# Optimization experiments

Measured on AMD Instinct MI355X. Metric: run time of the kernel, lower is better.

The kernel has to match this reference:

```python
import jax, jax.numpy as jnp
import numpy as np

N = 4096          # number of bodies
DIM = 2           # 2D physics (Parallax robot soccer)
K_BROAD = 4 * N   # broad phase keeps first 4N AABB overlaps (per source)
K_EXACT = N       # exact phase keeps first N true penetrations (per source)


def setup_inputs() -> dict:
    key = jax.random.key(0)
    k1, k2 = jax.random.split(key)
    # disk bodies scattered in a ~160x160 arena -> dense enough for many hits
    pos = jax.random.normal(k1, (N, DIM), dtype=jnp.float32) * 40.0
    radius = jax.random.uniform(k2, (N,), dtype=jnp.float32, minval=0.5, maxval=1.5)
    return {"pos": pos, "radius": radius}


def _forward(pos, radius):
    n = pos.shape[0]
    # ---- broad phase: sphere AABB = pos +- radius; two boxes overlap iff
    # |p_i - p_j| <= r_i + r_j on every axis. Full O(N^2) scan (as in source),
    # compact the first K_BROAD hits in row-major (i*n + j) order.
    d = jnp.abs(pos[:, None, :] - pos[None, :, :])            # [N,N,DIM]
    rsum = radius[:, None] + radius[None, :]                  # [N,N]
    overlap = jnp.all(d <= rsum[..., None], axis=-1)          # [N,N] bool
    overlap = overlap & ~jnp.eye(n, dtype=bool)               # skip self-pairs
    flat = overlap.reshape(-1)                                # [N*N]
    rank = jnp.cumsum(flat.astype(jnp.int32)) - 1             # slot of each hit
    valid = flat & (rank < K_BROAD)
    slot = jnp.where(valid, rank, K_BROAD)                    # K_BROAD -> dropped
    ii = jnp.repeat(jnp.arange(n, dtype=jnp.int32), n)
    jj = jnp.tile(jnp.arange(n, dtype=jnp.int32), n)
    bi = jnp.full((K_BROAD,), -1, jnp.int32).at[slot].set(ii, mode='drop')
    bj = jnp.full((K_BROAD,), -1, jnp.int32).at[slot].set(jj, mode='drop')
    # ---- exact phase: sphere-sphere penetration test on broad pairs,
    # keep first K_EXACT real penetrations (gather-compute-compact).
    gi = jnp.clip(bi, 0, n - 1)
    gj = jnp.clip(bj, 0, n - 1)
    dv = pos[gi] - pos[gj]                                    # [K_BROAD,DIM]
    dist = jnp.sqrt(jnp.sum(dv * dv, axis=-1) + 1e-12)
    pen_depth = radius[gi] + radius[gj] - dist                # >0 means overlap
    hit = (bi >= 0) & (pen_depth > 0)
    erank = jnp.cumsum(hit.astype(jnp.int32)) - 1
    evalid = hit & (erank < K_EXACT)
    eslot = jnp.where(evalid, erank, K_EXACT)                 # K_EXACT -> dropped
    pen_vec = dv * (pen_depth / dist)[:, None]                # penetration vector
    ei = jnp.full((K_EXACT,), -1, jnp.int32).at[eslot].set(bi, mode='drop')
    ej = jnp.full((K_EXACT,), -1, jnp.int32).at[eslot].set(bj, mode='drop')
    ev = jnp.zeros((K_EXACT, pos.shape[-1]), pos.dtype).at[eslot].set(pen_vec, mode='drop')
    # ---- resolve: each body of the pair is pushed half the penetration apart,
    si = jnp.where(ei >= 0, ei, n)                            # n -> dropped
    sj = jnp.where(ej >= 0, ej, n)
    new_i = pos[jnp.clip(ei, 0, n - 1)] + 0.5 * ev
    new_j = pos[jnp.clip(ej, 0, n - 1)] - 0.5 * ev
    out = pos.at[si].set(new_i, mode='drop')
    out = out.at[sj].set(new_j, mode='drop')
    return out


def reference(pos, radius):
    return _forward(pos, radius)
```

## Files before the change

kernel.cpp:

```cpp
#include <hip/hip_runtime.h>

#define NB 4096
#define KBROAD (4 * NB)
#define KEXACT NB
typedef unsigned long long u64;

__global__ __launch_bounds__(256) void count_kernel(
    const float2* __restrict__ pos, const float* __restrict__ rad,
    int* __restrict__ row_counts, u64* __restrict__ masks,
    int* __restrict__ last_key) {
  int gid = blockIdx.x * blockDim.x + threadIdx.x;
  if (gid < NB) last_key[gid] = -1;
  int wave = gid >> 6;
  int lane = gid & 63;
  int r0 = wave * 2;
  float2 p0 = pos[r0], p1 = pos[r0 + 1];
  float ra0 = rad[r0], ra1 = rad[r0 + 1];
  int cc = r0 >> 6;
  u64 mw0 = 0, mw1 = 0;
  int c0 = 0, c1 = 0;
  for (int c = 0; c < 64; ++c) {
    int j = c * 64 + lane;
    float2 pj = pos[j];
    float rj = rad[j];
    bool h0 = fmaxf(fabsf(p0.x - pj.x), fabsf(p0.y - pj.y)) <= (ra0 + rj);
    bool h1 = fmaxf(fabsf(p1.x - pj.x), fabsf(p1.y - pj.y)) <= (ra1 + rj);
    u64 m0 = __ballot(h0);
    u64 m1 = __ballot(h1);
    if (c == cc) {
      m0 &= ~(1ull << (r0 & 63));
      m1 &= ~(1ull << ((r0 + 1) & 63));
    }
    if (lane == c) { mw0 = m0; mw1 = m1; }
    c0 += __popcll(m0);
    c1 += __popcll(m1);
  }
  masks[(size_t)r0 * 64 + lane] = mw0;
  masks[(size_t)(r0 + 1) * 64 + lane] = mw1;
  if (lane == 0) { row_counts[r0] = c0; row_counts[r0 + 1] = c1; }
}

__global__ __launch_bounds__(256) void fill_kernel(
    const float2* __restrict__ pos, const float* __restrict__ rad,
    const int* __restrict__ row_counts, const u64* __restrict__ masks,
    float2* __restrict__ penvec, unsigned* __restrict__ pij,
    int* __restrict__ totalp) {
  __shared__ int rb[NB];
  __shared__ int wsum[4];
  int t = threadIdx.x;
  int wv = t >> 6, lane = t & 63;
  int c[16], s = 0;
  const int4* rc4 = (const int4*)row_counts;
  #pragma unroll
  for (int k4 = 0; k4 < 4; ++k4) {
    int4 d = rc4[t * 4 + k4];
    c[4 * k4 + 0] = d.x; c[4 * k4 + 1] = d.y;
    c[4 * k4 + 2] = d.z; c[4 * k4 + 3] = d.w;
    s += d.x + d.y + d.z + d.w;
  }
  int v = s;
  #pragma unroll
  for (int off = 1; off < 64; off <<= 1) {
    int u = __shfl_up(v, off);
    if (lane >= off) v += u;
  }
  if (lane == 63) wsum[wv] = v;
  __syncthreads();
  int wbase = 0;
  #pragma unroll
  for (int w = 0; w < 4; ++w) if (w < wv) wbase += wsum[w];
  int run = wbase + v - s;
  #pragma unroll
  for (int k = 0; k < 16; ++k) { rb[k * 256 + t] = run; run += c[k]; }
  if (blockIdx.x == 0 && t == 255) totalp[0] = run;
  __syncthreads();
  for (int q = 0; q < 4; ++q) {
    int r = blockIdx.x * 16 + wv * 4 + q;
    int rowbase = rb[(r & 15) * 256 + (r >> 4)];
    if (rowbase >= KBROAD) continue;
    u64 myw = masks[(size_t)r * 64 + lane];
    int cnt = __popcll(myw);
    int v2 = cnt;
    #pragma unroll
    for (int off = 1; off < 64; off <<= 1) {
      int u = __shfl_up(v2, off);
      if (lane >= off) v2 += u;
    }
    int rank = rowbase + v2 - cnt;
    if (!myw) continue;
    float2 pr = pos[r];
    float rr = rad[r];
    u64 m = myw;
    while (m && rank < KBROAD) {
      int b = __builtin_ctzll(m);
      m &= m - 1;
      int j = (lane << 6) + b;
      float2 pj = pos[j];
      float dx = pr.x - pj.x, dy = pr.y - pj.y;
      float ss = __fadd_rn(__fadd_rn(__fmul_rn(dx, dx), __fmul_rn(dy, dy)), 1e-12f);
      float dist = __fsqrt_rn(ss);
      float pen = __fsub_rn(__fadd_rn(rr, rad[j]), dist);
      if (pen > 0.0f) {
        float sc = __fdiv_rn(pen, dist);
        penvec[rank] = make_float2(__fmul_rn(dx, sc), __fmul_rn(dy, sc));
        pij[rank] = ((unsigned)r << 16) | (unsigned)j;
      }
      ++rank;
    }
  }
}

__global__ __launch_bounds__(256) void exact_kernel(
    const unsigned* __restrict__ pij, const float2* __restrict__ penvec,
    const int* __restrict__ totalp, float2* __restrict__ ev,
    int* __restrict__ last_key) {
  __shared__ u64 bm[256];
  __shared__ int eb[256];
  __shared__ int wsum[4];
  int t = threadIdx.x;
  int wv = t >> 6, lane = t & 63;
  int total = totalp[0];
  if (total > KBROAD) total = KBROAD;
  u64 m = 0;
  int base = t * 64;
  #pragma unroll
  for (int k = 0; k < 16; ++k) {
    uint4 d = ((const uint4*)pij)[t * 16 + k];
    int s = base + 4 * k;
    unsigned n = 0;
    n |= (((d.x & 0xF000F000u) == 0u) && (s + 0 < total)) ? 1u : 0u;
    n |= (((d.y & 0xF000F000u) == 0u) && (s + 1 < total)) ? 2u : 0u;
    n |= (((d.z & 0xF000F000u) == 0u) && (s + 2 < total)) ? 4u : 0u;
    n |= (((d.w & 0xF000F000u) == 0u) && (s + 3 < total)) ? 8u : 0u;
    m |= (u64)n << (4 * k);
  }
  int cnt = __popcll(m);
  int v = cnt;
  #pragma unroll
  for (int off = 1; off < 64; off <<= 1) {
    int u = __shfl_up(v, off);
    if (lane >= off) v += u;
  }
  if (lane == 63) wsum[wv] = v;
  bm[t] = m;
  __syncthreads();
  int wbase = 0;
  #pragma unroll
  for (int w = 0; w < 4; ++w) if (w < wv) wbase += wsum[w];
  eb[t] = wbase + v - cnt;
  __syncthreads();
  int s = blockIdx.x * 256 + t;
  u64 w = bm[s >> 6];
  if ((w >> (s & 63)) & 1ull) {
    int rank = eb[s >> 6] + __popcll(w & (((u64)1 << (s & 63)) - 1ull));
    if (rank < KEXACT) {
      ev[rank] = penvec[s];
      unsigned p = pij[s];
      atomicMax(&last_key[p >> 16], rank);
      atomicMax(&last_key[p & 0xFFFFu], 0x10000 | rank);
    }
  }
}

__global__ __launch_bounds__(256) void combine_kernel(
    const float2* __restrict__ pos, const int* __restrict__ last_key,
    const float2* __restrict__ ev, float2* __restrict__ out) {
  int b = blockIdx.x * blockDim.x + threadIdx.x;
  float2 p = pos[b];
  int k = last_key[b];
  float2 o = p;
  if (k >= 0) {
    int rank = k & 0xFFFF;
    float2 e = ev[rank];
    if (k & 0x10000) {
      o.x = __fsub_rn(p.x, __fmul_rn(0.5f, e.x));
      o.y = __fsub_rn(p.y, __fmul_rn(0.5f, e.y));
    } else {
      o.x = __fadd_rn(p.x, __fmul_rn(0.5f, e.x));
      o.y = __fadd_rn(p.y, __fmul_rn(0.5f, e.y));
    }
  }
  out[b] = o;
}

extern "C" void kernel_launch(void* const* d_in, const int* in_sizes, int n_in,
                              void* d_out, int out_size, void* d_ws, size_t ws_size,
                              hipStream_t stream) {
  const float2* pos = (const float2*)d_in[0];
  const float* rad = (const float*)d_in[1];
  float2* out = (float2*)d_out;

  unsigned* pij = (unsigned*)d_ws;
  float2* penvec = (float2*)(pij + KBROAD);
  float2* ev = penvec + KBROAD;
  u64* masks = (u64*)(ev + KEXACT);
  int* row_counts = (int*)(masks + (size_t)NB * 64);
  int* totalp = row_counts + NB;
  int* last_key = totalp + 1;

  count_kernel<<<512, 256, 0, stream>>>(pos, rad, row_counts, masks, last_key);
  fill_kernel<<<256, 256, 0, stream>>>(pos, rad, row_counts, masks, penvec,
                                       pij, totalp);
  exact_kernel<<<64, 256, 0, stream>>>(pij, penvec, totalp, ev, last_key);
  combine_kernel<<<16, 256, 0, stream>>>(pos, last_key, ev, out);
}
```

Baseline: 81.46 us.

## Split count rows across waves and hierarchical prefix via per-block sums

The count kernel now has each wave test 4 rows against half the columns, with two waves per row group. This raises per-load reuse of column bodies and cuts the serial loop length from 64 to 32 iterations. Each block also writes a per-8-row partial sum, so the fill kernel can compute row bases from 512 block sums plus 16 local row counts instead of scanning all 4096 row counts in every block. The cost is an extra shared-memory reduction and barrier in the count kernel, plus more registers per thread.

Result: no change. 82.65 us (+1.5%).

```diff
diff --git a/kernel.cpp b/kernel.cpp
--- a/kernel.cpp
+++ b/kernel.cpp
@@ -8,75 +8,109 @@
 __global__ __launch_bounds__(256) void count_kernel(
     const float2* __restrict__ pos, const float* __restrict__ rad,
     int* __restrict__ row_counts, u64* __restrict__ masks,
-    int* __restrict__ last_key) {
+    int* __restrict__ blocksum8, int* __restrict__ last_key) {
+  __shared__ int ws[4][4];
   int gid = blockIdx.x * blockDim.x + threadIdx.x;
   if (gid < NB) last_key[gid] = -1;
-  int wave = gid >> 6;
-  int lane = gid & 63;
-  int r0 = wave * 2;
-  float2 p0 = pos[r0], p1 = pos[r0 + 1];
-  float ra0 = rad[r0], ra1 = rad[r0 + 1];
+  int t = threadIdx.x;
+  int wv = t >> 6, lane = t & 63;
+  int g = wv >> 1;
+  int h = wv & 1;
+  int r0 = blockIdx.x * 8 + g * 4;
+  float2 p0 = pos[r0], p1 = pos[r0 + 1], p2 = pos[r0 + 2], p3 = pos[r0 + 3];
+  float ra0 = rad[r0], ra1 = rad[r0 + 1], ra2 = rad[r0 + 2], ra3 = rad[r0 + 3];
   int cc = r0 >> 6;
-  u64 mw0 = 0, mw1 = 0;
-  int c0 = 0, c1 = 0;
-  for (int c = 0; c < 64; ++c) {
+  u64 mw0 = 0, mw1 = 0, mw2 = 0, mw3 = 0;
+  int c0 = 0, c1 = 0, c2 = 0, c3 = 0;
+  #pragma unroll 2
+  for (int ci = 0; ci < 32; ++ci) {
+    int c = h * 32 + ci;
     int j = c * 64 + lane;
     float2 pj = pos[j];
     float rj = rad[j];
     bool h0 = fmaxf(fabsf(p0.x - pj.x), fabsf(p0.y - pj.y)) <= (ra0 + rj);
     bool h1 = fmaxf(fabsf(p1.x - pj.x), fabsf(p1.y - pj.y)) <= (ra1 + rj);
+    bool h2 = fmaxf(fabsf(p2.x - pj.x), fabsf(p2.y - pj.y)) <= (ra2 + rj);
+    bool h3 = fmaxf(fabsf(p3.x - pj.x), fabsf(p3.y - pj.y)) <= (ra3 + rj);
     u64 m0 = __ballot(h0);
     u64 m1 = __ballot(h1);
+    u64 m2 = __ballot(h2);
+    u64 m3 = __ballot(h3);
     if (c == cc) {
       m0 &= ~(1ull << (r0 & 63));
       m1 &= ~(1ull << ((r0 + 1) & 63));
-    }
-    if (lane == c) { mw0 = m0; mw1 = m1; }
+      m2 &= ~(1ull << ((r0 + 2) & 63));
+      m3 &= ~(1ull << ((r0 + 3) & 63));
+    }
+    if (lane == ci) { mw0 = m0; mw1 = m1; mw2 = m2; mw3 = m3; }
     c0 += __popcll(m0);
     c1 += __popcll(m1);
-  }
-  masks[(size_t)r0 * 64 + lane] = mw0;
-  masks[(size_t)(r0 + 1) * 64 + lane] = mw1;
-  if (lane == 0) { row_counts[r0] = c0; row_counts[r0 + 1] = c1; }
+    c2 += __popcll(m2);
+    c3 += __popcll(m3);
+  }
+  if (lane < 32) {
+    size_t base = (size_t)r0 * 64 + h * 32 + lane;
+    masks[base] = mw0;
+    masks[base + 64] = mw1;
+    masks[base + 128] = mw2;
+    masks[base + 192] = mw3;
+  }
+  if (lane == 0) { ws[wv][0] = c0; ws[wv][1] = c1; ws[wv][2] = c2; ws[wv][3] = c3; }
+  __syncthreads();
+  if (t < 8) {
+    int gg = t >> 2, k = t & 3;
+    row_counts[blockIdx.x * 8 + gg * 4 + k] = ws[2 * gg][k] + ws[2 * gg + 1][k];
+  }
+  if (t == 0) {
+    int s = 0;
+    #pragma unroll
+    for (int w = 0; w < 4; ++w) s += ws[w][0] + ws[w][1] + ws[w][2] + ws[w][3];
+    blocksum8[blockIdx.x] = s;
+  }
 }
 
 __global__ __launch_bounds__(256) void fill_kernel(
     const float2* __restrict__ pos, const float* __restrict__ rad,
-    const int* __restrict__ row_counts, const u64* __restrict__ masks,
+    const int* __restrict__ row_counts, const int* __restrict__ blocksum8,
+    const u64* __restrict__ masks,
     float2* __restrict__ penvec, unsigned* __restrict__ pij,
     int* __restrict__ totalp) {
-  __shared__ int rb[NB];
-  __shared__ int wsum[4];
+  __shared__ int rbase[16];
   int t = threadIdx.x;
   int wv = t >> 6, lane = t & 63;
-  int c[16], s = 0;
-  const int4* rc4 = (const int4*)row_counts;
-  #pragma unroll
-  for (int k4 = 0; k4 < 4; ++k4) {
-    int4 d = rc4[t * 4 + k4];
-    c[4 * k4 + 0] = d.x; c[4 * k4 + 1] = d.y;
-    c[4 * k4 + 2] = d.z; c[4 * k4 + 3] = d.w;
-    s += d.x + d.y + d.z + d.w;
-  }
-  int v = s;
-  #pragma unroll
-  for (int off = 1; off < 64; off <<= 1) {
-    int u = __shfl_up(v, off);
-    if (lane >= off) v += u;
-  }
-  if (lane == 63) wsum[wv] = v;
-  __syncthreads();
-  int wbase = 0;
-  #pragma unroll
-  for (int w = 0; w < 4; ++w) if (w < wv) wbase += wsum[w];
-  int run = wbase + v - s;
-  #pragma unroll
-  for (int k = 0; k < 16; ++k) { rb[k * 256 + t] = run; run += c[k]; }
-  if (blockIdx.x == 0 && t == 255) totalp[0] = run;
+  int b = blockIdx.x;
+  if (wv == 0) {
+    const int4* bs4 = (const int4*)blocksum8;
+    int4 d0 = bs4[lane * 2];
+    int4 d1 = bs4[lane * 2 + 1];
+    int s = d0.x + d0.y + d0.z + d0.w + d1.x + d1.y + d1.z + d1.w;
+    int v = s;
+    #pragma unroll
+    for (int off = 1; off < 64; off <<= 1) {
+      int u = __shfl_up(v, off);
+      if (lane >= off) v += u;
+    }
+    int excl = v - s;
+    int m = (2 * b) & 7;
+    int inner = 0;
+    if (m > 0) inner += d0.x + d0.y;
+    if (m > 2) inner += d0.z + d0.w;
+    if (m > 4) inner += d1.x + d1.y;
+    int P = __shfl(excl + inner, b >> 2);
+    if (b == 0 && lane == 63) totalp[0] = v;
+    int cnt = (lane < 16) ? row_counts[16 * b + lane] : 0;
+    int vv = cnt;
+    #pragma unroll
+    for (int off = 1; off < 16; off <<= 1) {
+      int u = __shfl_up(vv, off);
+      if (lane >= off) vv += u;
+    }
+    if (lane < 16) rbase[lane] = P + vv - cnt;
+  }
   __syncthreads();
   for (int q = 0; q < 4; ++q) {
-    int r = blockIdx.x * 16 + wv * 4 + q;
-    int rowbase = rb[(r & 15) * 256 + (r >> 4)];
+    int r = b * 16 + wv * 4 + q;
+    int rowbase = rbase[wv * 4 + q];
     if (rowbase >= KBROAD) continue;
     u64 myw = masks[(size_t)r * 64 + lane];
     int cnt = __popcll(myw);
@@ -92,9 +126,9 @@
     float rr = rad[r];
     u64 m = myw;
     while (m && rank < KBROAD) {
-      int b = __builtin_ctzll(m);
+      int b2 = __builtin_ctzll(m);
       m &= m - 1;
-      int j = (lane << 6) + b;
+      int j = (lane << 6) + b2;
       float2 pj = pos[j];
       float dx = pr.x - pj.x, dy = pr.y - pj.y;
       float ss = __fadd_rn(__fadd_rn(__fmul_rn(dx, dx), __fmul_rn(dy, dy)), 1e-12f);
@@ -195,12 +229,14 @@
   float2* ev = penvec + KBROAD;
   u64* masks = (u64*)(ev + KEXACT);
   int* row_counts = (int*)(masks + (size_t)NB * 64);
-  int* totalp = row_counts + NB;
+  int* blocksum8 = row_counts + NB;
+  int* totalp = blocksum8 + 512;
   int* last_key = totalp + 1;
 
-  count_kernel<<<512, 256, 0, stream>>>(pos, rad, row_counts, masks, last_key);
-  fill_kernel<<<256, 256, 0, stream>>>(pos, rad, row_counts, masks, penvec,
-                                       pij, totalp);
+  count_kernel<<<512, 256, 0, stream>>>(pos, rad, row_counts, masks,
+                                        blocksum8, last_key);
+  fill_kernel<<<256, 256, 0, stream>>>(pos, rad, row_counts, blocksum8, masks,
+                                       penvec, pij, totalp);
   exact_kernel<<<64, 256, 0, stream>>>(pij, penvec, totalp, ev, last_key);
   combine_kernel<<<16, 256, 0, stream>>>(pos, last_key, ev, out);
 }
```
